# Performance work log

Hardware: AMD Instinct MI355X
Metric: run time of the kernel (lower is better)

Reference implementation:

```python
import jax, jax.numpy as jnp
import numpy as np

N_NODES = 100000
N_EDGES = 1600000
F_IN = 128
D_OUT = 64
BN_EPS = 1e-3  # keras BatchNormalization default epsilon
LRELU_SLOPE = 0.2  # tf.nn.leaky_relu default alpha


def setup_inputs() -> dict:
    key = jax.random.key(0)
    ks = jax.random.split(key, 6)
    x = jax.random.normal(ks[0], (N_NODES, F_IN), dtype=jnp.float32)
    src = jax.random.randint(ks[1], (N_EDGES,), 0, N_NODES, dtype=jnp.int32)
    dst = jax.random.randint(ks[2], (N_EDGES,), 0, N_NODES, dtype=jnp.int32)
    adj_vals = jnp.ones((N_EDGES,), dtype=jnp.float32)
    W = jax.random.normal(ks[3], (F_IN, D_OUT), dtype=jnp.float32)
    K1 = jax.random.normal(ks[4], (F_IN, F_IN), dtype=jnp.float32)
    K2 = jax.random.normal(ks[5], (F_IN, F_IN), dtype=jnp.float32)
    return {"x": x, "src": src, "dst": dst, "adj_vals": adj_vals, "W": W, "K1": K1, "K2": K2}


def reference(x, src, dst, adj_vals, W, K1, K2):
    n = x.shape[0]
    # training-mode batch norm over the node (batch) axis, gamma=1, beta=0
    mean = jnp.mean(x, axis=0)
    var = jnp.var(x, axis=0)
    xn = (x - mean) * jax.lax.rsqrt(var + BN_EPS)
    mapped = xn @ W                                   # [N, D]
    a1 = jnp.tanh(jnp.sum((xn @ K1) * xn, axis=1))    # [N] row scalar
    a2 = jnp.tanh(jnp.sum((xn @ K2) * xn, axis=1))    # [N] col scalar
    # edge score e_ij = leaky_relu(v_ij*a1[i] + v_ij*a2[j])
    e = jax.nn.leaky_relu(adj_vals * (a1[src] + a2[dst]), negative_slope=LRELU_SLOPE)
    # per-row (src) sparse softmax
    emax = jax.ops.segment_max(e, src, num_segments=n)
    ee = jnp.exp(e - emax[src])
    denom = jax.ops.segment_sum(ee, src, num_segments=n)
    attn = ee / denom[src]                            # [E]
    # SpMM: out[i] = sum_j attn_ij * mapped[j]
    out = jax.ops.segment_sum(attn[:, None] * mapped[dst], src, num_segments=n)
    return jnp.tanh(out)
```

## Files before the change

### kernel.cpp

```cpp
#include <hip/hip_runtime.h>
#include <hip/hip_fp16.h>
#include <math.h>

#define F_IN 128
#define D_OUT 64
#define LRELU 0.2f
#define BN_EPS 1e-3f
#define XPITCH 136
#define NB 391
#define CHA 2048
#define CAPB 6144
#define NBLK 128

typedef __attribute__((ext_vector_type(8))) __bf16 bf16x8;
typedef __attribute__((ext_vector_type(4))) __bf16 bf16x4;
typedef __attribute__((ext_vector_type(4))) float f32x4;

__global__ __launch_bounds__(256) void stats_kernel(const float* __restrict__ x,
                                                    float* __restrict__ sum,
                                                    float* __restrict__ sumsq,
                                                    int N, int rowsPerBlock) {
    __shared__ float lsum[8][132], lsq[8][132];
    int tid  = threadIdx.x;
    int c4   = (tid & 31) * 4;
    int rgrp = tid >> 5;
    int rbeg = blockIdx.x * rowsPerBlock;
    int rend = min(rbeg + rowsPerBlock, N);
    float sx = 0.f, sy = 0.f, sz = 0.f, sw = 0.f;
    float qx = 0.f, qy = 0.f, qz = 0.f, qw = 0.f;
    for (int r = rbeg + rgrp; r < rend; r += 8) {
        float4 v = *(const float4*)&x[(size_t)r * F_IN + c4];
        sx += v.x; sy += v.y; sz += v.z; sw += v.w;
        qx += v.x * v.x; qy += v.y * v.y; qz += v.z * v.z; qw += v.w * v.w;
    }
    lsum[rgrp][c4] = sx; lsum[rgrp][c4 + 1] = sy;
    lsum[rgrp][c4 + 2] = sz; lsum[rgrp][c4 + 3] = sw;
    lsq[rgrp][c4] = qx; lsq[rgrp][c4 + 1] = qy;
    lsq[rgrp][c4 + 2] = qz; lsq[rgrp][c4 + 3] = qw;
    __syncthreads();
    if (tid < 128) {
        float a = 0.f, b = 0.f;
#pragma unroll
        for (int g = 0; g < 8; ++g) { a += lsum[g][tid]; b += lsq[g][tid]; }
        atomicAdd(&sum[tid], a);
        atomicAdd(&sumsq[tid], b);
    }
}

__global__ void finalize_stats(float* sum, float* sumsq, int N) {
    int c = threadIdx.x;
    float mean = sum[c] / (float)N;
    float var  = sumsq[c] / (float)N - mean * mean;
    sum[c]   = mean;
    sumsq[c] = rsqrtf(var + BN_EPS);
}

__global__ __launch_bounds__(256) void prep_B(const float* __restrict__ K1,
                                              const float* __restrict__ K2,
                                              const float* __restrict__ W,
                                              __bf16* __restrict__ Bth,
                                              __bf16* __restrict__ Btl) {
    int i = blockIdx.x * 256 + threadIdx.x;
    if (i >= 320 * 128) return;
    int c = i >> 7, k = i & 127;
    float v;
    if (c < 128)      v = K1[k * 128 + c];
    else if (c < 256) v = K2[k * 128 + (c - 128)];
    else              v = W[k * 64 + (c - 256)];
    __bf16 h = (__bf16)v;
    int ct = c >> 4, col16 = c & 15;
    int ks = k >> 5, quad = (k >> 3) & 3, e = k & 7;
    int off = ct * 2048 + ks * 512 + (quad * 16 + col16) * 8 + e;
    Bth[off] = h;
    Btl[off] = (__bf16)(v - (float)h);
}

__global__ __launch_bounds__(256, 2) void node_kernel(const float* __restrict__ x,
                                                      const __bf16* __restrict__ Bth,
                                                      const __bf16* __restrict__ Btl,
                                                      const float* __restrict__ meanv,
                                                      const float* __restrict__ rstdv,
                                                      float* __restrict__ a1,
                                                      float* __restrict__ a2,
                                                      __half* __restrict__ mapped,
                                                      int N) {
    __shared__ __bf16 xh[64][XPITCH];
    __shared__ __bf16 xl[64][XPITCH];
    __shared__ float mS[128], rS[128];
    __shared__ float paA[4][64], paB[4][64];

    int tid   = threadIdx.x;
    int lane  = tid & 63;
    int w     = tid >> 6;
    int col16 = lane & 15;
    int quad  = lane >> 4;
    int kb    = quad * 8;

    if (tid < 128) { mS[tid] = meanv[tid]; rS[tid] = rstdv[tid]; }
    __syncthreads();

    int base = blockIdx.x * 64;

#pragma unroll
    for (int it = 0; it < 8; ++it) {
        int chunk = tid + it * 256;
        int r = chunk >> 5, c4 = (chunk & 31) * 4;
        int row = base + r;
        float f0 = 0.f, f1 = 0.f, f2 = 0.f, f3 = 0.f;
        if (row < N) {
            float4 v  = *(const float4*)&x[(size_t)row * F_IN + c4];
            float4 m  = *(const float4*)&mS[c4];
            float4 rs = *(const float4*)&rS[c4];
            f0 = (v.x - m.x) * rs.x; f1 = (v.y - m.y) * rs.y;
            f2 = (v.z - m.z) * rs.z; f3 = (v.w - m.w) * rs.w;
        }
        __bf16 h0 = (__bf16)f0, h1 = (__bf16)f1, h2 = (__bf16)f2, h3 = (__bf16)f3;
        bf16x4 hv = {h0, h1, h2, h3};
        bf16x4 lv = {(__bf16)(f0 - (float)h0), (__bf16)(f1 - (float)h1),
                     (__bf16)(f2 - (float)h2), (__bf16)(f3 - (float)h3)};
        *(bf16x4*)&xh[r][c4] = hv;
        *(bf16x4*)&xl[r][c4] = lv;
    }
    __syncthreads();

    float pa1[4] = {0, 0, 0, 0}, pa2[4] = {0, 0, 0, 0};

#pragma unroll
    for (int i = 0; i < 5; ++i) {
        int ct = w * 5 + i;
        const __bf16* ph = Bth + ct * 2048 + lane * 8;
        const __bf16* pl = Btl + ct * 2048 + lane * 8;
        bf16x8 Bh[4], Bl[4];
#pragma unroll
        for (int ks = 0; ks < 4; ++ks) {
            Bh[ks] = *(const bf16x8*)(ph + ks * 512);
            Bl[ks] = *(const bf16x8*)(pl + ks * 512);
        }
        bool isK  = (ct < 16);
        bool isA1 = (ct < 8);
        int cg = (ct & 7) * 16 + quad * 4;
        int cw = (ct - 16) * 16 + quad * 4;
#pragma unroll
        for (int rt = 0; rt < 4; ++rt) {
            int arow = rt * 16 + col16;
            bf16x8 Ah[4], Al[4];
#pragma unroll
            for (int ks = 0; ks < 4; ++ks) {
                Ah[ks] = *(bf16x8*)&xh[arow][ks * 32 + kb];
                Al[ks] = *(bf16x8*)&xl[arow][ks * 32 + kb];
            }
            f32x4 accA = {0, 0, 0, 0}, accB = {0, 0, 0, 0}, accC = {0, 0, 0, 0};
#pragma unroll
            for (int ks = 0; ks < 4; ++ks) {
                accA = __builtin_amdgcn_mfma_f32_16x16x32_bf16(Bh[ks], Ah[ks], accA, 0, 0, 0);
                accB = __builtin_amdgcn_mfma_f32_16x16x32_bf16(Bh[ks], Al[ks], accB, 0, 0, 0);
                accC = __builtin_amdgcn_mfma_f32_16x16x32_bf16(Bl[ks], Ah[ks], accC, 0, 0, 0);
            }
            f32x4 accT = accA + accB + accC;
            if (isK) {
                bf16x4 xh4 = *(bf16x4*)&xh[arow][cg];
                bf16x4 xl4 = *(bf16x4*)&xl[arow][cg];
                float s = accT[0] * ((float)xh4[0] + (float)xl4[0])
                        + accT[1] * ((float)xh4[1] + (float)xl4[1])
                        + accT[2] * ((float)xh4[2] + (float)xl4[2])
                        + accT[3] * ((float)xh4[3] + (float)xl4[3]);
                if (isA1) pa1[rt] += s; else pa2[rt] += s;
            } else {
                int node = base + arow;
                if (node < N) {
                    __half2 h01 = __floats2half2_rn(accT[0], accT[1]);
                    __half2 h23 = __floats2half2_rn(accT[2], accT[3]);
                    __half2* mp = (__half2*)&mapped[(size_t)node * 64 + cw];
                    mp[0] = h01; mp[1] = h23;
                }
            }
        }
    }

#pragma unroll
    for (int rt = 0; rt < 4; ++rt) {
        float v1 = pa1[rt], v2 = pa2[rt];
        v1 += __shfl_xor(v1, 16, 64); v1 += __shfl_xor(v1, 32, 64);
        v2 += __shfl_xor(v2, 16, 64); v2 += __shfl_xor(v2, 32, 64);
        if (quad == 0) {
            paA[w][rt * 16 + col16] = v1;
            paB[w][rt * 16 + col16] = v2;
        }
    }
    __syncthreads();
    if (tid < 64) {
        int node = base + tid;
        if (node < N) {
            a1[node] = tanhf(paA[0][tid] + paA[1][tid] + paA[2][tid] + paA[3][tid]);
            a2[node] = tanhf(paB[0][tid] + paB[1][tid] + paB[2][tid] + paB[3][tid]);
        }
    }
}

__global__ __launch_bounds__(256) void bhist_kernel(const int* __restrict__ src,
                                                    int* __restrict__ partial, int E) {
    __shared__ int h[NB];
    for (int b = threadIdx.x; b < NB; b += 256) h[b] = 0;
    __syncthreads();
    int per = (E + NBLK - 1) / NBLK;
    int beg = blockIdx.x * per;
    int end = min(beg + per, E);
    for (int e = beg + threadIdx.x; e < end; e += 256)
        atomicAdd(&h[src[e] >> 8], 1);
    __syncthreads();
    for (int b = threadIdx.x; b < NB; b += 256)
        partial[blockIdx.x * NB + b] = h[b];
}

__global__ __launch_bounds__(512) void bscan_kernel(const int* __restrict__ partial,
                                                    int* __restrict__ bcur,
                                                    int* __restrict__ bscan,
                                                    int* __restrict__ rowptr,
                                                    int N, int E) {
    __shared__ int s[512];
    int b = threadIdx.x;
    int sum = 0;
    if (b < NB)
        for (int r = 0; r < NBLK; ++r) sum += partial[r * NB + b];
    s[b] = sum;
    for (int off = 1; off < 512; off <<= 1) {
        __syncthreads();
        int t = (b >= off) ? s[b - off] : 0;
        __syncthreads();
        s[b] += t;
    }
    __syncthreads();
    int excl = s[b] - sum;
    if (b < NB) { bcur[b] = excl; bscan[b] = excl; }
    if (b == 0) { bscan[NB] = E; rowptr[N] = E; }
}

__global__ __launch_bounds__(256) void binA_kernel(const int* __restrict__ src,
                                                   const int* __restrict__ dst,
                                                   const float* __restrict__ adj,
                                                   const float* __restrict__ a1,
                                                   const float* __restrict__ a2,
                                                   int* __restrict__ bcur,
                                                   int2* __restrict__ sorted, int E) {
    __shared__ int2 listL[CHA];
    __shared__ int  addrL[CHA];
    __shared__ int  scan0[NB], scanW[NB], curL[NB];
    __shared__ int  tsum[256];
    int tid = threadIdx.x;
    int ebase = blockIdx.x * CHA;
    int count = min(CHA, E - ebase);

    for (int b = tid; b < NB; b += 256) scanW[b] = 0;
    __syncthreads();
    for (int i = tid; i < count; i += 256)
        atomicAdd(&scanW[src[ebase + i] >> 8], 1);
    __syncthreads();
    int b0 = tid * 2, b1 = tid * 2 + 1;
    int v0 = (b0 < NB) ? scanW[b0] : 0;
    int v1 = (b1 < NB) ? scanW[b1] : 0;
    tsum[tid] = v0 + v1;
    for (int off = 1; off < 256; off <<= 1) {
        __syncthreads();
        int t = (tid >= off) ? tsum[tid - off] : 0;
        __syncthreads();
        tsum[tid] += t;
    }
    __syncthreads();
    int excl = tsum[tid] - v0 - v1;
    if (b0 < NB) scan0[b0] = excl;
    if (b1 < NB) scan0[b1] = excl + v0;
    __syncthreads();
    for (int b = tid; b < NB; b += 256) {
        int c = scanW[b];
        if (c > 0) curL[b] = atomicAdd(&bcur[b], c);
        scanW[b] = scan0[b];
    }
    __syncthreads();
    for (int i = tid; i < count; i += 256) {
        int e = ebase + i;
        int s = src[e], d = dst[e];
        float v = adj[e] * (a1[s] + a2[d]);
        v = (v > 0.f) ? v : LRELU * v;
        float ex = __expf(v);
        int b = s >> 8;
        int p = atomicAdd(&scanW[b], 1);
        listL[p] = make_int2(((s & 255) << 24) | d, __float_as_int(ex));
        addrL[p] = curL[b] + (p - scan0[b]);
    }
    __syncthreads();
    for (int i = tid; i < count; i += 256)
        sorted[addrL[i]] = listL[i];
}

__global__ __launch_bounds__(256) void binB_kernel(const int* __restrict__ bscan,
                                                   int2* __restrict__ sorted,
                                                   int* __restrict__ rowptr, int N) {
    __shared__ int2 inL[CAPB];
    __shared__ int2 outL[CAPB];
    __shared__ int  c0[257], cW[256];
    int b   = blockIdx.x;
    int lo  = b << 8;
    int bbase = bscan[b];
    int len   = bscan[b + 1] - bbase;
    len = min(len, CAPB);
    int tid = threadIdx.x;
    cW[tid] = 0;
    __syncthreads();
    for (int i = tid; i < len; i += 256) {
        int2 pe = sorted[bbase + i];
        inL[i] = pe;
        atomicAdd(&cW[((unsigned)pe.x) >> 24], 1);
    }
    __syncthreads();
    if (tid == 0) {
        int run = 0;
        for (int k = 0; k < 256; ++k) { int c = cW[k]; c0[k] = run; run += c; }
    }
    __syncthreads();
    if (lo + tid < N) rowptr[lo + tid] = bbase + c0[tid];
    cW[tid] = c0[tid];
    __syncthreads();
    for (int i = tid; i < len; i += 256) {
        int2 pe = inL[i];
        unsigned u = (unsigned)pe.x;
        int p = atomicAdd(&cW[u >> 24], 1);
        outL[p] = make_int2((int)(u & 0xFFFFFF), pe.y);
    }
    __syncthreads();
    for (int i = tid; i < len; i += 256)
        sorted[bbase + i] = outL[i];
}

#define SPMM_ACC(P, G)                                        \
    {                                                         \
        float wg = __int_as_float(P.y);                       \
        accw += wg;                                           \
        float2 m0 = __half22float2(*(__half2*)&G.x);          \
        float2 m1 = __half22float2(*(__half2*)&G.y);          \
        float2 m2 = __half22float2(*(__half2*)&G.z);          \
        float2 m3 = __half22float2(*(__half2*)&G.w);          \
        acc0 += wg * m0.x; acc1 += wg * m0.y;                 \
        acc2 += wg * m1.x; acc3 += wg * m1.y;                 \
        acc4 += wg * m2.x; acc5 += wg * m2.y;                 \
        acc6 += wg * m3.x; acc7 += wg * m3.y;                 \
    }

__global__ __launch_bounds__(256) void spmm_kernel(const int* __restrict__ rowptr,
                                                   const int2* __restrict__ sorted,
                                                   const __half2* __restrict__ mapped,
                                                   float* __restrict__ out, int N) {
    __shared__ float accL[8][64];
    __shared__ float accwL[8];
    int tid  = threadIdx.x;
    int w    = tid >> 6;
    int lane = tid & 63;
    int half = lane >> 5;
    int slot = (lane >> 3) & 3;
    int c    = lane & 7;
    int nl   = w * 2 + half;
    int node = blockIdx.x * 8 + nl;
    int beg = 0, end = 0;
    if (node < N) { beg = rowptr[node]; end = rowptr[node + 1]; }

    float acc0 = 0.f, acc1 = 0.f, acc2 = 0.f, acc3 = 0.f;
    float acc4 = 0.f, acc5 = 0.f, acc6 = 0.f, acc7 = 0.f;
    float accw = 0.f;
    const char* mb = (const char*)mapped;

    for (int chunk = beg; chunk < end; chunk += 16) {
        int e0 = chunk + slot;
        int2 p0 = (e0      < end) ? sorted[e0]      : make_int2(0, 0);
        int2 p1 = (e0 + 4  < end) ? sorted[e0 + 4]  : make_int2(0, 0);
        int2 p2 = (e0 + 8  < end) ? sorted[e0 + 8]  : make_int2(0, 0);
        int2 p3 = (e0 + 12 < end) ? sorted[e0 + 12] : make_int2(0, 0);
        int4 g0 = *(const int4*)(mb + (((unsigned)p0.x << 7) | (c << 4)));
        int4 g1 = *(const int4*)(mb + (((unsigned)p1.x << 7) | (c << 4)));
        int4 g2 = *(const int4*)(mb + (((unsigned)p2.x << 7) | (c << 4)));
        int4 g3 = *(const int4*)(mb + (((unsigned)p3.x << 7) | (c << 4)));
        SPMM_ACC(p0, g0);
        SPMM_ACC(p1, g1);
        SPMM_ACC(p2, g2);
        SPMM_ACC(p3, g3);
    }

#pragma unroll
    for (int off = 8; off < 32; off <<= 1) {
        acc0 += __shfl_xor(acc0, off, 64);
        acc1 += __shfl_xor(acc1, off, 64);
        acc2 += __shfl_xor(acc2, off, 64);
        acc3 += __shfl_xor(acc3, off, 64);
        acc4 += __shfl_xor(acc4, off, 64);
        acc5 += __shfl_xor(acc5, off, 64);
        acc6 += __shfl_xor(acc6, off, 64);
        acc7 += __shfl_xor(acc7, off, 64);
        accw += __shfl_xor(accw, off, 64);
    }
    if (slot == 0) {
        float* al = &accL[nl][c * 8];
        al[0] = acc0; al[1] = acc1; al[2] = acc2; al[3] = acc3;
        al[4] = acc4; al[5] = acc5; al[6] = acc6; al[7] = acc7;
        if (c == 0) accwL[nl] = accw;
    }
    __syncthreads();

    int n    = tid >> 5;
    int col  = tid & 31;
    int node2 = blockIdx.x * 8 + n;
    if (node2 < N) {
        float aw  = accwL[n];
        float inv = (aw != 0.f) ? 1.f / aw : 0.f;
        float* op = &out[(size_t)node2 * 64];
        op[col]      = tanhf(accL[n][col] * inv);
        op[col + 32] = tanhf(accL[n][col + 32] * inv);
    }
}

extern "C" void kernel_launch(void* const* d_in, const int* in_sizes, int n_in,
                              void* d_out, int out_size, void* d_ws, size_t ws_size,
                              hipStream_t stream) {
    const float* x   = (const float*)d_in[0];
    const int*   src = (const int*)d_in[1];
    const int*   dst = (const int*)d_in[2];
    const float* adj = (const float*)d_in[3];
    const float* W   = (const float*)d_in[4];
    const float* K1  = (const float*)d_in[5];
    const float* K2  = (const float*)d_in[6];
    float* out = (float*)d_out;

    const int N = in_sizes[0] / F_IN;
    const int E = in_sizes[1];

    float* meanv  = (float*)d_ws;
    float* rstdv  = meanv + 128;
    float* a1     = rstdv + 128;
    float* a2     = a1 + N;
    __half* mapped = (__half*)(a2 + N);
    int*   rowptr = (int*)(mapped + (size_t)N * 64);
    int*   bscan  = rowptr + (N + 1);
    int*   bcur   = bscan + (NB + 1);
    int*   partial = bcur + NB;
    uintptr_t sp  = ((uintptr_t)(partial + NBLK * NB) + 15) & ~(uintptr_t)15;
    int2*  sorted = (int2*)sp;
    __bf16* Bth   = (__bf16*)(sorted + E);
    __bf16* Btl   = Bth + 320 * 128;

    hipMemsetAsync(d_ws, 0, 256 * sizeof(float), stream);

    bhist_kernel<<<NBLK, 256, 0, stream>>>(src, partial, E);

    int rpb = (N + 511) / 512;
    stats_kernel<<<512, 256, 0, stream>>>(x, meanv, rstdv, N, rpb);
    finalize_stats<<<1, 128, 0, stream>>>(meanv, rstdv, N);

    prep_B<<<(320 * 128 + 255) / 256, 256, 0, stream>>>(K1, K2, W, Bth, Btl);

    node_kernel<<<(N + 63) / 64, 256, 0, stream>>>(x, Bth, Btl, meanv, rstdv,
                                                   a1, a2, mapped, N);

    bscan_kernel<<<1, 512, 0, stream>>>(partial, bcur, bscan, rowptr, N, E);

    binA_kernel<<<(E + CHA - 1) / CHA, 256, 0, stream>>>(src, dst, adj, a1, a2,
                                                         bcur, sorted, E);
    binB_kernel<<<NB, 256, 0, stream>>>(bscan, sorted, rowptr, N);

    spmm_kernel<<<(N + 7) / 8, 256, 0, stream>>>(rowptr, sorted,
                                                 (const __half2*)mapped, out, N);
}
```

Before: 321.6 us.

## Precompute per-block bucket offsets to replace global atomics in edge binning

The bucket histogram is now computed per binning chunk (782 blocks instead of 128). A new kernel, bscan2, scans those per-block counts within each bucket to produce deterministic per-block base offsets. binA no longer rebuilds its local histogram or takes global atomics on the bucket cursors, and reads the precomputed counts and bases instead. This removes a pass over src in binA and the global atomic contention, at the cost of one extra small kernel launch and a larger partial array that bscan must sum. bscan2 holds at most 8 values per thread in a local array, which caps nblkA at 2048.

Measured after the change: 390.8 us. 1.22x slower.

```diff
diff --git a/kernel.cpp b/kernel.cpp
--- a/kernel.cpp
+++ b/kernel.cpp
@@ -10,7 +10,6 @@
 #define NB 391
 #define CHA 2048
 #define CAPB 6144
-#define NBLK 128
 
 typedef __attribute__((ext_vector_type(8))) __bf16 bf16x8;
 typedef __attribute__((ext_vector_type(4))) __bf16 bf16x4;
@@ -202,9 +201,8 @@
     __shared__ int h[NB];
     for (int b = threadIdx.x; b < NB; b += 256) h[b] = 0;
     __syncthreads();
-    int per = (E + NBLK - 1) / NBLK;
-    int beg = blockIdx.x * per;
-    int end = min(beg + per, E);
+    int beg = blockIdx.x * CHA;
+    int end = min(beg + CHA, E);
     for (int e = beg + threadIdx.x; e < end; e += 256)
         atomicAdd(&h[src[e] >> 8], 1);
     __syncthreads();
@@ -213,15 +211,14 @@
 }
 
 __global__ __launch_bounds__(512) void bscan_kernel(const int* __restrict__ partial,
-                                                    int* __restrict__ bcur,
                                                     int* __restrict__ bscan,
                                                     int* __restrict__ rowptr,
-                                                    int N, int E) {
+                                                    int N, int E, int nblkA) {
     __shared__ int s[512];
     int b = threadIdx.x;
     int sum = 0;
     if (b < NB)
-        for (int r = 0; r < NBLK; ++r) sum += partial[r * NB + b];
+        for (int r = 0; r < nblkA; ++r) sum += partial[r * NB + b];
     s[b] = sum;
     for (int off = 1; off < 512; off <<= 1) {
         __syncthreads();
@@ -230,9 +227,39 @@
         s[b] += t;
     }
     __syncthreads();
-    int excl = s[b] - sum;
-    if (b < NB) { bcur[b] = excl; bscan[b] = excl; }
+    if (b < NB) bscan[b] = s[b] - sum;
     if (b == 0) { bscan[NB] = E; rowptr[N] = E; }
+}
+
+__global__ __launch_bounds__(256) void bscan2_kernel(const int* __restrict__ partial,
+                                                     const int* __restrict__ bscan,
+                                                     int* __restrict__ baseT,
+                                                     int nblkA) {
+    __shared__ int tsum[256];
+    int b   = blockIdx.x;
+    int tid = threadIdx.x;
+    int per = (nblkA + 255) / 256;
+    int lv[8];
+    int r0 = tid * per;
+    int mysum = 0;
+    for (int i = 0; i < per; ++i) {
+        int r = r0 + i;
+        lv[i] = (r < nblkA) ? partial[r * NB + b] : 0;
+        mysum += lv[i];
+    }
+    tsum[tid] = mysum;
+    for (int off = 1; off < 256; off <<= 1) {
+        __syncthreads();
+        int t = (tid >= off) ? tsum[tid - off] : 0;
+        __syncthreads();
+        tsum[tid] += t;
+    }
+    __syncthreads();
+    int run = bscan[b] + tsum[tid] - mysum;
+    for (int i = 0; i < per; ++i) {
+        int r = r0 + i;
+        if (r < nblkA) { baseT[r * NB + b] = run; run += lv[i]; }
+    }
 }
 
 __global__ __launch_bounds__(256) void binA_kernel(const int* __restrict__ src,
@@ -240,24 +267,21 @@
                                                    const float* __restrict__ adj,
                                                    const float* __restrict__ a1,
                                                    const float* __restrict__ a2,
-                                                   int* __restrict__ bcur,
+                                                   const int* __restrict__ partial,
+                                                   const int* __restrict__ baseT,
                                                    int2* __restrict__ sorted, int E) {
     __shared__ int2 listL[CHA];
     __shared__ int  addrL[CHA];
     __shared__ int  scan0[NB], scanW[NB], curL[NB];
     __shared__ int  tsum[256];
     int tid = threadIdx.x;
-    int ebase = blockIdx.x * CHA;
+    int blk = blockIdx.x;
+    int ebase = blk * CHA;
     int count = min(CHA, E - ebase);
 
-    for (int b = tid; b < NB; b += 256) scanW[b] = 0;
-    __syncthreads();
-    for (int i = tid; i < count; i += 256)
-        atomicAdd(&scanW[src[ebase + i] >> 8], 1);
-    __syncthreads();
     int b0 = tid * 2, b1 = tid * 2 + 1;
-    int v0 = (b0 < NB) ? scanW[b0] : 0;
-    int v1 = (b1 < NB) ? scanW[b1] : 0;
+    int v0 = (b0 < NB) ? partial[blk * NB + b0] : 0;
+    int v1 = (b1 < NB) ? partial[blk * NB + b1] : 0;
     tsum[tid] = v0 + v1;
     for (int off = 1; off < 256; off <<= 1) {
         __syncthreads();
@@ -267,15 +291,10 @@
     }
     __syncthreads();
     int excl = tsum[tid] - v0 - v1;
-    if (b0 < NB) scan0[b0] = excl;
-    if (b1 < NB) scan0[b1] = excl + v0;
-    __syncthreads();
-    for (int b = tid; b < NB; b += 256) {
-        int c = scanW[b];
-        if (c > 0) curL[b] = atomicAdd(&bcur[b], c);
-        scanW[b] = scan0[b];
-    }
-    __syncthreads();
+    if (b0 < NB) { scan0[b0] = excl; scanW[b0] = excl; curL[b0] = baseT[blk * NB + b0]; }
+    if (b1 < NB) { scan0[b1] = excl + v0; scanW[b1] = excl + v0; curL[b1] = baseT[blk * NB + b1]; }
+    __syncthreads();
+
     for (int i = tid; i < count; i += 256) {
         int e = ebase + i;
         int s = src[e], d = dst[e];
@@ -429,6 +448,7 @@
 
     const int N = in_sizes[0] / F_IN;
     const int E = in_sizes[1];
+    const int nblkA = (E + CHA - 1) / CHA;
 
     float* meanv  = (float*)d_ws;
     float* rstdv  = meanv + 128;
@@ -437,16 +457,16 @@
     __half* mapped = (__half*)(a2 + N);
     int*   rowptr = (int*)(mapped + (size_t)N * 64);
     int*   bscan  = rowptr + (N + 1);
-    int*   bcur   = bscan + (NB + 1);
-    int*   partial = bcur + NB;
-    uintptr_t sp  = ((uintptr_t)(partial + NBLK * NB) + 15) & ~(uintptr_t)15;
+    int*   partial = bscan + (NB + 1);
+    int*   baseT   = partial + (size_t)nblkA * NB;
+    uintptr_t sp  = ((uintptr_t)(baseT + (size_t)nblkA * NB) + 15) & ~(uintptr_t)15;
     int2*  sorted = (int2*)sp;
     __bf16* Bth   = (__bf16*)(sorted + E);
     __bf16* Btl   = Bth + 320 * 128;
 
     hipMemsetAsync(d_ws, 0, 256 * sizeof(float), stream);
 
-    bhist_kernel<<<NBLK, 256, 0, stream>>>(src, partial, E);
+    bhist_kernel<<<nblkA, 256, 0, stream>>>(src, partial, E);
 
     int rpb = (N + 511) / 512;
     stats_kernel<<<512, 256, 0, stream>>>(x, meanv, rstdv, N, rpb);
@@ -457,10 +477,11 @@
     node_kernel<<<(N + 63) / 64, 256, 0, stream>>>(x, Bth, Btl, meanv, rstdv,
                                                    a1, a2, mapped, N);
 
-    bscan_kernel<<<1, 512, 0, stream>>>(partial, bcur, bscan, rowptr, N, E);
-
-    binA_kernel<<<(E + CHA - 1) / CHA, 256, 0, stream>>>(src, dst, adj, a1, a2,
-                                                         bcur, sorted, E);
+    bscan_kernel<<<1, 512, 0, stream>>>(partial, bscan, rowptr, N, E, nblkA);
+    bscan2_kernel<<<NB, 256, 0, stream>>>(partial, bscan, baseT, nblkA);
+
+    binA_kernel<<<nblkA, 256, 0, stream>>>(src, dst, adj, a1, a2,
+                                           partial, baseT, sorted, E);
     binB_kernel<<<NB, 256, 0, stream>>>(bscan, sorted, rowptr, N);
 
     spmm_kernel<<<(N + 7) / 8, 256, 0, stream>>>(rowptr, sorted,
```
